# Performance work log

Measured on AMD Instinct MI355X. Metric: run time of the kernel, lower is better.

Reference implementation:

```python
import jax, jax.numpy as jnp
import numpy as np

B, T, D = 2, 4096, 1024
HD, HQ, KVH, W = 128, 8, 1, 1024   # head_dim, q_heads, kv_heads, window
HH, HG, K = 1536, 2048, 4          # hawk hidden, gmlp hidden, conv kernel
ALPHA_SCALE = float(np.log(8.0))   # alpha_log_scale (stored as log, used exp'd)


def setup_inputs() -> dict:
    key = jax.random.key(0)
    ks = jax.random.split(key, 16)
    n = lambda k, shape, std: jax.random.normal(k, shape, jnp.float32) * std
    return {
        'x': n(ks[0], (B, T, D), 1.0),
        'sn_g': jnp.ones((D,), jnp.float32),
        'q_w': n(ks[1], (HQ * HD, D), D ** -0.5),
        'kv_w': n(ks[2], (2 * KVH * HD, D), D ** -0.5),
        'ao_w': n(ks[3], (D, D), D ** -0.5),
        'sgn_g': jnp.ones((D,), jnp.float32),
        'sg_grow': n(ks[4], (2 * HG, D), D ** -0.5),
        'sg_shrink': n(ks[5], (D, HG), HG ** -0.5),
        'hn_g': jnp.ones((D,), jnp.float32),
        'h_in_w': n(ks[6], (2 * HH, D), D ** -0.5),
        'h_conv_w': n(ks[7], (HH, 1, K), K ** -0.5),
        'h_conv_b': jnp.zeros((HH,), jnp.float32),
        'h_gates_w': n(ks[8], (2 * HH, HH), HH ** -0.5),
        'h_gates_b': jnp.zeros((2 * HH,), jnp.float32),
        'h_forget': jnp.linspace(-4.323, -9.0, HH, dtype=jnp.float32),
        'h_out_w': n(ks[9], (D, HH), HH ** -0.5),
        'hgn_g': jnp.ones((D,), jnp.float32),
        'hg_grow': n(ks[10], (2 * HG, D), D ** -0.5),
        'hg_shrink': n(ks[11], (D, HG), HG ** -0.5),
    }


def rmsnorm(x, gamma):
    # original: gamma / dim**-0.5 * x / ||x||_2  (no eps)
    inv = jax.lax.rsqrt(jnp.sum(x * x, axis=-1, keepdims=True))
    return gamma * (x.shape[-1] ** 0.5) * x * inv


def rope(x, base=10000.0):
    # x: (B, T, H, HD); interleaved rotary over time axis 1
    t = x.shape[1]
    hd = x.shape[-1]
    inv = 1.0 / (base ** (jnp.arange(0, hd, 2, dtype=jnp.float32) / hd))
    ang = jnp.arange(t, dtype=jnp.float32)[:, None] * inv[None, :]  # (T, HD/2)
    cos = jnp.cos(ang)[None, :, None, :]
    sin = jnp.sin(ang)[None, :, None, :]
    x1, x2 = x[..., 0::2], x[..., 1::2]
    y1 = x1 * cos - x2 * sin
    y2 = x1 * sin + x2 * cos
    return jnp.stack([y1, y2], axis=-1).reshape(x.shape)


def sliding_mqa(x, q_w, kv_w, ao_w):
    # MQA with causal sliding window of W, computed in blocks of W
    q = (x @ q_w.T).reshape(B, T, HQ, HD)
    kv = (x @ kv_w.T).reshape(B, T, 2, KVH, HD)
    k = kv[:, :, 0, 0]  # (B, T, HD) since KVH == 1
    v = kv[:, :, 1, 0]
    q = rope(q)
    k = rope(k[:, :, None, :])[:, :, 0]
    nb = T // W
    qb = q.reshape(B, nb, W, HQ, HD)
    kb = k.reshape(B, nb, W, HD)
    vb = v.reshape(B, nb, W, HD)
    # prepend previous block (zeros for block 0)
    shift = lambda a: jnp.concatenate([jnp.zeros_like(a[:, :1]), a[:, :-1]], axis=1)
    k2 = jnp.concatenate([shift(kb), kb], axis=2)  # (B, nb, 2W, HD)
    v2 = jnp.concatenate([shift(vb), vb], axis=2)
    qi = jnp.arange(W)[:, None]
    kj = jnp.arange(2 * W)[None, :]
    base = (kj >= qi) & (kj <= qi + W)  # causal + window (i-j <= W)
    blk0 = base & (kj >= W)             # block 0 has no real previous block
    mask = jnp.where(jnp.arange(nb)[:, None, None] == 0, blk0[None], base[None])
    scores = jnp.einsum('bnqhd,bnkd->bhnqk', qb, k2) * (HD ** -0.5)
    scores = jnp.where(mask[None, None], scores, -jnp.inf)
    p = jax.nn.softmax(scores, axis=-1)
    o = jnp.einsum('bhnqk,bnkd->bnqhd', p, v2).reshape(B, T, HQ * HD)
    return o @ ao_w.T


def gated_mlp(x, grow_w, shrink_w):
    gate, h = jnp.split(x @ grow_w.T, 2, axis=-1)
    return (jax.nn.gelu(gate, approximate=False) * h) @ shrink_w.T


def hawk(x, in_w, conv_w, conv_b, gates_w, gates_b, forget_base, out_w):
    gate, u = jnp.split(x @ in_w.T, 2, axis=-1)  # (B, T, HH) each
    # depthwise causal conv1d (torch pads k-1 both sides then slices [:T])
    u_nch = jnp.transpose(u, (0, 2, 1))  # (B, HH, T)
    c = jax.lax.conv_general_dilated(
        u_nch, conv_w, window_strides=(1,), padding=[(K - 1, 0)],
        feature_group_count=HH, dimension_numbers=('NCH', 'OIH', 'NCH'))
    xc = jnp.transpose(c + conv_b[None, :, None], (0, 2, 1))  # (B, T, HH)
    fg, ig = jnp.split(xc @ gates_w.T + gates_b, 2, axis=-1)
    log_alpha = -np.exp(ALPHA_SCALE) * jax.nn.softplus(forget_base) * jax.nn.sigmoid(fg)
    alpha = jnp.exp(log_alpha)
    beta = jnp.sqrt(1.0 - alpha * alpha + 1e-6)
    xin = beta * jax.nn.sigmoid(ig) * xc
    # linear recurrence h_t = alpha_t * h_{t-1} + xin_t  via associative scan
    def combine(c1, c2):
        a1, x1 = c1
        a2, x2 = c2
        return a1 * a2, a2 * x1 + x2
    _, h = jax.lax.associative_scan(combine, (alpha, xin), axis=1)
    return (jax.nn.gelu(gate, approximate=False) * h) @ out_w.T


def reference(x, sn_g, q_w, kv_w, ao_w, sgn_g, sg_grow, sg_shrink,
              hn_g, h_in_w, h_conv_w, h_conv_b, h_gates_w, h_gates_b,
              h_forget, h_out_w, hgn_g, hg_grow, hg_shrink):
    x = x + sliding_mqa(rmsnorm(x, sn_g), q_w, kv_w, ao_w)
    x = x + gated_mlp(rmsnorm(x, sgn_g), sg_grow, sg_shrink)
    x = x + hawk(rmsnorm(x, hn_g), h_in_w, h_conv_w, h_conv_b,
                 h_gates_w, h_gates_b, h_forget, h_out_w)
    x = x + gated_mlp(rmsnorm(x, hgn_g), hg_grow, hg_shrink)
    return x
```

## Files before the change

### kernel.cpp

```cpp
#include <hip/hip_runtime.h>
#include <hip/hip_bf16.h>
#include <math.h>

#define B_  2
#define T_  4096
#define D_  1024
#define HD_ 128
#define HQ_ 8
#define W_  1024
#define HH_ 1536
#define HG_ 2048
#define KC_ 4

typedef float  f32x4  __attribute__((ext_vector_type(4)));
typedef float  f32x2  __attribute__((ext_vector_type(2)));
typedef __bf16 bf16x8 __attribute__((ext_vector_type(8)));
typedef unsigned short u16;
typedef unsigned short u16x2 __attribute__((ext_vector_type(2)));
typedef unsigned short u16x4 __attribute__((ext_vector_type(4)));
typedef unsigned short u16x8 __attribute__((ext_vector_type(8)));

__device__ __forceinline__ u16 f2bf(float f) {
    unsigned int u = __builtin_bit_cast(unsigned int, f);
    u += 0x7fffu + ((u >> 16) & 1u);
    return (u16)(u >> 16);
}
__device__ __forceinline__ float bf2f(u16 v) {
    unsigned int u = ((unsigned int)v) << 16;
    return __builtin_bit_cast(float, u);
}
__device__ __forceinline__ float gelu_exact(float x) {
    return 0.5f * x * (1.0f + erff(x * 0.70710678118654752f));
}
__device__ __forceinline__ float sigmoidf_(float x) {
    return 1.0f / (1.0f + expf(-x));
}

#define GLOAD16(gp, lp) __builtin_amdgcn_global_load_lds( \
    (const __attribute__((address_space(1))) void*)(gp),  \
    (__attribute__((address_space(3))) void*)(lp), 16, 0, 0)

struct CvtArgs {
    const float* src[10];
    u16* dst[10];
    long cum[11];
};
__global__ __launch_bounds__(256)
void cvt_all_kernel(CvtArgs a)
{
    long i = ((long)blockIdx.x * 256 + threadIdx.x) * 8;
    if (i >= a.cum[10]) return;
    int seg = 0;
#pragma unroll
    for (int s = 1; s < 10; s++) if (i >= a.cum[s]) seg = s;
    long off = i - a.cum[seg];
    const float* src = a.src[seg];
    u16* dst = a.dst[seg];
    f32x4 x = *(const f32x4*)(src + off);
    f32x4 y = *(const f32x4*)(src + off + 4);
    u16x4 ua, ub;
    ua.x = f2bf(x.x); ua.y = f2bf(x.y); ua.z = f2bf(x.z); ua.w = f2bf(x.w);
    ub.x = f2bf(y.x); ub.y = f2bf(y.y); ub.z = f2bf(y.z); ub.w = f2bf(y.w);
    *(u16x4*)(dst + off) = ua;
    *(u16x4*)(dst + off + 4) = ub;
}

template<int EPI, bool OBF>
__global__ __launch_bounds__(512)
void gemm_big_kernel(const u16* __restrict__ A, const u16* __restrict__ Bw,
                     const float* __restrict__ bias, const float* __restrict__ res,
                     const u16* gatebuf, void* outv,
                     int M, int N, int K)
{
    __shared__ u16 lA[3][256 * 32];
    __shared__ u16 lB[3][128 * 32];
    const int n0 = blockIdx.x * 128, m0 = blockIdx.y * 256;
    const int tid = threadIdx.x, w = tid >> 6, l = tid & 63;
    const int wr = w >> 1, wc = w & 1;
    const int lr = l & 15, lg = l >> 4;

    f32x4 acc[4][4];
#pragma unroll
    for (int i = 0; i < 4; i++)
#pragma unroll
        for (int j = 0; j < 4; j++) acc[i][j] = {0.f, 0.f, 0.f, 0.f};

    const int srow = tid >> 2;
    const int gslot = (((tid) & 3) - ((tid >> 3) & 3)) & 3;
    const u16* gA = A + (long)(m0 + srow) * K + gslot * 8;
    const u16* gB = Bw + (long)(n0 + srow) * K + gslot * 8;
    const int lofs = tid * 8;

#define STAGE_G(buf, kk)                                            \
    {                                                               \
        GLOAD16(gA + (kk),                 &lA[buf][lofs]);         \
        GLOAD16(gA + (long)128 * K + (kk), &lA[buf][4096 + lofs]);  \
        GLOAD16(gB + (kk),                 &lB[buf][lofs]);         \
    }

    const int NT = K >> 5;
    STAGE_G(0, 0);
    STAGE_G(1, 32);

    const int swzr = (lr >> 1) & 3;
    int cur = 0;
    for (int t = 0; t < NT; ++t) {
        if (t == NT - 1) { asm volatile("s_waitcnt vmcnt(0)" ::: "memory"); }
        else             { asm volatile("s_waitcnt vmcnt(3)" ::: "memory"); }
        __builtin_amdgcn_s_barrier();
        __builtin_amdgcn_sched_barrier(0);
        if (t + 2 < NT) {
            int nb = cur + 2; if (nb >= 3) nb -= 3;
            STAGE_G(nb, (t + 2) << 5);
        }
        bf16x8 af[4], bfr[4];
#pragma unroll
        for (int m = 0; m < 4; m++)
            af[m] = *(const bf16x8*)&lA[cur][(wr * 64 + m * 16 + lr) * 32 + (((lg + swzr) & 3) * 8)];
#pragma unroll
        for (int n = 0; n < 4; n++)
            bfr[n] = *(const bf16x8*)&lB[cur][(wc * 64 + n * 16 + lr) * 32 + (((lg + swzr) & 3) * 8)];
        __builtin_amdgcn_s_setprio(1);
#pragma unroll
        for (int m = 0; m < 4; m++)
#pragma unroll
            for (int n = 0; n < 4; n++)
                acc[m][n] = __builtin_amdgcn_mfma_f32_16x16x32_bf16(af[m], bfr[n], acc[m][n], 0, 0, 0);
        __builtin_amdgcn_s_setprio(0);
        cur++; if (cur == 3) cur = 0;
    }
#undef STAGE_G

#pragma unroll
    for (int m = 0; m < 4; m++)
#pragma unroll
        for (int n = 0; n < 4; n++) {
            const int col = n0 + wc * 64 + n * 16 + lr;
            const float bv = (EPI == 1) ? bias[col] : 0.f;
#pragma unroll
            for (int r = 0; r < 4; r++) {
                const int row = m0 + wr * 64 + m * 16 + lg * 4 + r;
                const long idx = (long)row * N + col;
                float v = acc[m][n][r] + bv;
                if (EPI == 2) v += res[idx];
                if (EPI == 3) v = gelu_exact(bf2f(gatebuf[idx])) * v;
                if (OBF) ((u16*)outv)[idx] = f2bf(v);
                else     ((float*)outv)[idx] = v;
            }
        }
}

template<int EPI, bool OBF>
__global__ __launch_bounds__(256)
void gemm_bf16_kernel(const u16* __restrict__ A, const u16* __restrict__ Bw,
                      const float* __restrict__ bias, const float* __restrict__ res,
                      const u16* gatebuf, void* outv,
                      int M, int N, int K)
{
    __shared__ u16 lA[3][128 * 32];
    __shared__ u16 lB[3][128 * 32];
    const int n0 = blockIdx.x * 128, m0 = blockIdx.y * 128;
    const int tid = threadIdx.x, w = tid >> 6, l = tid & 63;
    const int wr = w >> 1, wc = w & 1, lr = l & 15, lg = l >> 4;

    f32x4 acc[4][4];
#pragma unroll
    for (int i = 0; i < 4; i++)
#pragma unroll
        for (int j = 0; j < 4; j++) acc[i][j] = {0.f, 0.f, 0.f, 0.f};

    const int srow = w * 16 + (l >> 2);
    const int gslot = ((l & 3) - ((l >> 3) & 3)) & 3;
    const u16* gA = A + (long)(m0 + srow) * K + gslot * 8;
    const u16* gB = Bw + (long)(n0 + srow) * K + gslot * 8;
    const int lofs = w * 512 + l * 8;

#define STAGE_G(buf, kk)                                          \
    {                                                             \
        GLOAD16(gA + (kk),                &lA[buf][lofs]);        \
        GLOAD16(gA + (long)64 * K + (kk), &lA[buf][2048 + lofs]); \
        GLOAD16(gB + (kk),                &lB[buf][lofs]);        \
        GLOAD16(gB + (long)64 * K + (kk), &lB[buf][2048 + lofs]); \
    }

    const int NT = K >> 5;
    STAGE_G(0, 0);
    STAGE_G(1, 32);

    const int swzr = (lr >> 1) & 3;
    int cur = 0;
    for (int t = 0; t < NT; ++t) {
        if (t == NT - 1) { asm volatile("s_waitcnt vmcnt(0)" ::: "memory"); }
        else             { asm volatile("s_waitcnt vmcnt(4)" ::: "memory"); }
        __builtin_amdgcn_s_barrier();
        __builtin_amdgcn_sched_barrier(0);
        if (t + 2 < NT) {
            int nb = cur + 2; if (nb >= 3) nb -= 3;
            STAGE_G(nb, (t + 2) << 5);
        }
        bf16x8 af[4], bfr[4];
#pragma unroll
        for (int m = 0; m < 4; m++)
            af[m] = *(const bf16x8*)&lA[cur][(wr * 64 + m * 16 + lr) * 32 + (((lg + swzr) & 3) * 8)];
#pragma unroll
        for (int n = 0; n < 4; n++)
            bfr[n] = *(const bf16x8*)&lB[cur][(wc * 64 + n * 16 + lr) * 32 + (((lg + swzr) & 3) * 8)];
        __builtin_amdgcn_s_setprio(1);
#pragma unroll
        for (int m = 0; m < 4; m++)
#pragma unroll
            for (int n = 0; n < 4; n++)
                acc[m][n] = __builtin_amdgcn_mfma_f32_16x16x32_bf16(af[m], bfr[n], acc[m][n], 0, 0, 0);
        __builtin_amdgcn_s_setprio(0);
        cur++; if (cur == 3) cur = 0;
    }
#undef STAGE_G

#pragma unroll
    for (int m = 0; m < 4; m++)
#pragma unroll
        for (int n = 0; n < 4; n++) {
            const int col = n0 + wc * 64 + n * 16 + lr;
            const float bv = (EPI == 1) ? bias[col] : 0.f;
#pragma unroll
            for (int r = 0; r < 4; r++) {
                const int row = m0 + wr * 64 + m * 16 + lg * 4 + r;
                const long idx = (long)row * N + col;
                float v = acc[m][n][r] + bv;
                if (EPI == 2) v += res[idx];
                if (EPI == 3) v = gelu_exact(bf2f(gatebuf[idx])) * v;
                if (OBF) ((u16*)outv)[idx] = f2bf(v);
                else     ((float*)outv)[idx] = v;
            }
        }
}

__global__ __launch_bounds__(256)
void rmsnorm_kernel(const float* __restrict__ x, const float* __restrict__ g,
                    u16* __restrict__ out)
{
    const long row = blockIdx.x;
    const int tid = threadIdx.x;
    const float* xp = x + row * D_;
    f32x4 v = *(const f32x4*)(xp + tid * 4);
    float ss = v.x * v.x + v.y * v.y + v.z * v.z + v.w * v.w;
#pragma unroll
    for (int o = 1; o < 64; o <<= 1) ss += __shfl_xor(ss, o);
    __shared__ float ps[4];
    if ((tid & 63) == 0) ps[tid >> 6] = ss;
    __syncthreads();
    float tot = ps[0] + ps[1] + ps[2] + ps[3];
    float inv = rsqrtf(tot) * 32.0f;
    f32x4 gv = *(const f32x4*)(g + tid * 4);
    u16x4 o4;
    o4.x = f2bf(gv.x * v.x * inv); o4.y = f2bf(gv.y * v.y * inv);
    o4.z = f2bf(gv.z * v.z * inv); o4.w = f2bf(gv.w * v.w * inv);
    *(u16x4*)(out + row * D_ + tid * 4) = o4;
}

__global__ void rope_bf16_kernel(const float* __restrict__ q, const float* __restrict__ kv,
                                 u16* __restrict__ qb, u16* __restrict__ kb)
{
    const long NQ = (long)B_ * T_ * HQ_ * 64;
    const long NK = (long)B_ * T_ * 64;
    long idx = (long)blockIdx.x * blockDim.x + threadIdx.x;
    if (idx >= NQ + NK) return;
    int i; long t; const float* src; u16* dst;
    if (idx < NQ) {
        i = idx & 63;
        long bth = idx >> 6;
        t = (bth / HQ_) % T_;
        src = q + bth * HD_ + 2 * i;
        dst = qb + bth * HD_ + 2 * i;
    } else {
        long k = idx - NQ;
        i = k & 63;
        long bt = k >> 6;
        t = bt % T_;
        src = kv + bt * (2 * HD_) + 2 * i;
        dst = kb + bt * HD_ + 2 * i;
    }
    float freq = exp2f(-(float)i * 0.20762050593046014f);
    float ang = (float)t * freq;
    float sn, cs;
    sincosf(ang, &sn, &cs);
    f32x2 xv = *(const f32x2*)src;
    u16x2 yv;
    yv.x = f2bf(xv.x * cs - xv.y * sn);
    yv.y = f2bf(xv.x * sn + xv.y * cs);
    *(u16x2*)dst = yv;
}

__global__ __launch_bounds__(256)
void vtrans_kernel(const float* __restrict__ kv, u16* __restrict__ vt)
{
    __shared__ float tile[64][65];
    const int t0 = blockIdx.x * 64, d0 = blockIdx.y * 64, b = blockIdx.z;
    const int tid = threadIdx.x;
    {
        const int tl = tid & 63, dg = tid >> 6;
        const float* vp = kv + (((long)b * T_ + t0 + tl) * 2 + 1) * HD_ + d0 + dg * 16;
#pragma unroll
        for (int j = 0; j < 4; j++) {
            f32x4 v = *(const f32x4*)(vp + j * 4);
            tile[dg * 16 + j * 4 + 0][tl] = v.x;
            tile[dg * 16 + j * 4 + 1][tl] = v.y;
            tile[dg * 16 + j * 4 + 2][tl] = v.z;
            tile[dg * 16 + j * 4 + 3][tl] = v.w;
        }
    }
    __syncthreads();
    {
        const int dl = tid >> 2, tg = (tid & 3) * 16;
        u16x8 a, c;
#pragma unroll
        for (int j = 0; j < 8; j++) a[j] = f2bf(tile[dl][tg + j]);
#pragma unroll
        for (int j = 0; j < 8; j++) c[j] = f2bf(tile[dl][tg + 8 + j]);
        u16* dst = vt + ((long)b * HD_ + d0 + dl) * T_ + t0 + tg;
        *(u16x8*)dst = a;
        *(u16x8*)(dst + 8) = c;
    }
}

#define PLD 72

__global__ __launch_bounds__(256)
void attn_mfma3_kernel(const u16* __restrict__ qb, const u16* __restrict__ kb,
                       const u16* __restrict__ vt, u16* __restrict__ o)
{
    __shared__ u16 Ksh[2][64 * 128];
    __shared__ u16 Vsh[2][128 * 64];
    __shared__ u16 Psh[4 * 16 * PLD];

    const int qt = blockIdx.x, h = blockIdx.y, b = blockIdx.z;
    const int q0 = qt * 64;
    const int tid = threadIdx.x;
    const int w = tid >> 6, l = tid & 63;
    const int lr = l & 15, lg = l >> 4;

    bf16x8 qfr[4];
    {
        const u16* qp = qb + (((long)b * T_ + q0 + w * 16 + lr) * HQ_ + h) * HD_;
#pragma unroll
        for (int kt = 0; kt < 4; kt++)
            qfr[kt] = *(const bf16x8*)(qp + kt * 32 + lg * 8);
    }

    int oK[4], oV[4];
#pragma unroll
    for (int i = 0; i < 4; i++) {
        int krow = w * 16 + i * 4 + (l >> 4);
        int kc8 = (l & 15) ^ (krow & 7);
        oK[i] = krow * 128 + kc8 * 8;
        int vrow = w * 32 + i * 8 + (l >> 3);
        int vc8 = (l & 7) ^ (vrow & 7);
        oV[i] = vrow * T_ + vc8 * 8;
    }
    const u16* kbase = kb + (long)b * T_ * HD_;
    const u16* vbase = vt + (long)b * HD_ * T_;

    f32x4 oacc[8];
#pragma unroll
    for (int dt = 0; dt < 8; dt++) oacc[dt] = {0.f, 0.f, 0.f, 0.f};
    float mrun[4], srun[4];
#pragma unroll
    for (int r = 0; r < 4; r++) { mrun[r] = -1e30f; srun[r] = 0.f; }

    const int kt_lo = (q0 >= W_) ? (q0 - W_) : 0;
    const int nt = ((q0 - kt_lo) >> 6) + 1;
    const int sw = lr & 7;
    const float scale = 0.08838834764831845f;

#pragma unroll
    for (int i = 0; i < 4; i++) {
        GLOAD16(kbase + (long)kt_lo * HD_ + oK[i], &Ksh[0][w * 2048 + i * 512]);
        GLOAD16(vbase + kt_lo + oV[i], &Vsh[0][w * 2048 + i * 512]);
    }

    for (int t = 0; t < nt; ++t) {
        const int kt0 = kt_lo + t * 64;
        const int cur = t & 1;
        if (t + 1 < nt) {
            const int ktn = kt0 + 64;
#pragma unroll
            for (int i = 0; i < 4; i++) {
                GLOAD16(kbase + (long)ktn * HD_ + oK[i], &Ksh[cur ^ 1][w * 2048 + i * 512]);
                GLOAD16(vbase + ktn + oV[i], &Vsh[cur ^ 1][w * 2048 + i * 512]);
            }
            asm volatile("s_waitcnt vmcnt(8)" ::: "memory");
        } else {
            asm volatile("s_waitcnt vmcnt(0)" ::: "memory");
        }
        __builtin_amdgcn_s_barrier();
        __builtin_amdgcn_sched_barrier(0);

        const u16* Kc = Ksh[cur];
        const u16* Vc = Vsh[cur];

        f32x4 s[4];
        __builtin_amdgcn_s_setprio(1);
#pragma unroll
        for (int ct = 0; ct < 4; ct++) {
            s[ct] = {0.f, 0.f, 0.f, 0.f};
#pragma unroll
            for (int kt = 0; kt < 4; kt++) {
                bf16x8 kf = *(const bf16x8*)&Kc[(ct * 16 + lr) * 128 + (((kt * 4 + lg) ^ sw) * 8)];
                s[ct] = __builtin_amdgcn_mfma_f32_16x16x32_bf16(qfr[kt], kf, s[ct], 0, 0, 0);
            }
        }
        __builtin_amdgcn_s_setprio(0);

        float tmax[4] = {-3e38f, -3e38f, -3e38f, -3e38f};
        if (kt0 == q0) {
#pragma unroll
            for (int ct = 0; ct < 4; ct++) {
                const int kpos = kt0 + ct * 16 + lr;
#pragma unroll
                for (int r = 0; r < 4; r++) {
                    const int qpos = q0 + w * 16 + lg * 4 + r;
                    float v = s[ct][r] * scale;
                    v = (kpos <= qpos) ? v : -3e38f;
                    s[ct][r] = v;
                    tmax[r] = fmaxf(tmax[r], v);
                }
            }
        } else if (kt0 == q0 - W_) {
#pragma unroll
            for (int ct = 0; ct < 4; ct++) {
                const int kpos = kt0 + ct * 16 + lr;
#pragma unroll
                for (int r = 0; r < 4; r++) {
                    const int qpos = q0 + w * 16 + lg * 4 + r;
                    float v = s[ct][r] * scale;
                    v = (kpos + W_ >= qpos) ? v : -3e38f;
                    s[ct][r] = v;
                    tmax[r] = fmaxf(tmax[r], v);
                }
            }
        } else {
#pragma unroll
            for (int ct = 0; ct < 4; ct++)
#pragma unroll
                for (int r = 0; r < 4; r++) {
                    float v = s[ct][r] * scale;
                    s[ct][r] = v;
                    tmax[r] = fmaxf(tmax[r], v);
                }
        }
#pragma unroll
        for (int r = 0; r < 4; r++)
#pragma unroll
            for (int msk = 1; msk < 16; msk <<= 1)
                tmax[r] = fmaxf(tmax[r], __shfl_xor(tmax[r], msk));

        bool defer = (tmax[0] <= mrun[0] + 8.f) && (tmax[1] <= mrun[1] + 8.f) &&
                     (tmax[2] <= mrun[2] + 8.f) && (tmax[3] <= mrun[3] + 8.f);
        if (!__all(defer)) {
            float frv[4];
#pragma unroll
            for (int r = 0; r < 4; r++) {
                float mnew = fmaxf(mrun[r], tmax[r]);
                frv[r] = __expf(mrun[r] - mnew);
                mrun[r] = mnew;
                srun[r] *= frv[r];
            }
#pragma unroll
            for (int dt = 0; dt < 8; dt++) {
                oacc[dt][0] *= frv[0]; oacc[dt][1] *= frv[1];
                oacc[dt][2] *= frv[2]; oacc[dt][3] *= frv[3];
            }
        }

        u16* pw = &Psh[w * 16 * PLD];
        float psum[4] = {0.f, 0.f, 0.f, 0.f};
#pragma unroll
        for (int ct = 0; ct < 4; ct++)
#pragma unroll
            for (int r = 0; r < 4; r++) {
                float p = __expf(s[ct][r] - mrun[r]);
                psum[r] += p;
                pw[(lg * 4 + r) * PLD + ct * 16 + lr] = f2bf(p);
            }
#pragma unroll
        for (int r = 0; r < 4; r++) {
#pragma unroll
            for (int msk = 1; msk < 16; msk <<= 1)
                psum[r] += __shfl_xor(psum[r], msk);
            srun[r] += psum[r];
        }

        asm volatile("s_waitcnt lgkmcnt(0)" ::: "memory");
        bf16x8 pa0 = *(const bf16x8*)&pw[lr * PLD + lg * 8];
        bf16x8 pa1 = *(const bf16x8*)&pw[lr * PLD + 32 + lg * 8];
        __builtin_amdgcn_s_setprio(1);
#pragma unroll
        for (int dt = 0; dt < 8; dt++) {
            bf16x8 vf0 = *(const bf16x8*)&Vc[(dt * 16 + lr) * 64 + ((lg ^ sw) * 8)];
            bf16x8 vf1 = *(const bf16x8*)&Vc[(dt * 16 + lr) * 64 + (((4 + lg) ^ sw) * 8)];
            oacc[dt] = __builtin_amdgcn_mfma_f32_16x16x32_bf16(pa0, vf0, oacc[dt], 0, 0, 0);
            oacc[dt] = __builtin_amdgcn_mfma_f32_16x16x32_bf16(pa1, vf1, oacc[dt], 0, 0, 0);
        }
        __builtin_amdgcn_s_setprio(0);
        __syncthreads();
    }

#pragma unroll
    for (int r = 0; r < 4; r++) {
        const int qpos = q0 + w * 16 + lg * 4 + r;
        float inv = 1.f / srun[r];
        u16* op = o + ((long)b * T_ + qpos) * (HQ_ * HD_) + h * HD_;
#pragma unroll
        for (int dt = 0; dt < 8; dt++)
            op[dt * 16 + lr] = f2bf(oacc[dt][r] * inv);
    }
}

__global__ void conv_kernel(const u16* __restrict__ u, const float* __restrict__ w,
                            const float* __restrict__ bias, u16* __restrict__ xc)
{
    long idx = (long)blockIdx.x * blockDim.x + threadIdx.x;
    if (idx >= (long)B_ * T_ * HH_) return;
    int ch = (int)(idx % HH_);
    long row = idx / HH_;
    int t = (int)(row % T_);
    float acc = bias[ch];
#pragma unroll
    for (int k = 0; k < KC_; k++) {
        int ts = t - 3 + k;
        if (ts >= 0) acc += bf2f(u[(row - t + ts) * HH_ + ch]) * w[ch * KC_ + k];
    }
    xc[idx] = f2bf(acc);
}

#define CS_ 64
#define NC_ (T_ / CS_)

__device__ __forceinline__ void alpha_xin(const u16 fg, const u16 ig, const u16 xc,
                                          float sp, float& a, float& xin)
{
    a = expf(-8.0f * sp * sigmoidf_(bf2f(fg)));
    xin = sqrtf(1.f - a * a + 1e-6f) * sigmoidf_(bf2f(ig)) * bf2f(xc);
}

__global__ void scan1_kernel(const u16* __restrict__ fg, const u16* __restrict__ ig,
                             const u16* __restrict__ xc, const float* __restrict__ fb,
                             float* __restrict__ P, float* __restrict__ L)
{
    long idx = (long)blockIdx.x * blockDim.x + threadIdx.x;
    if (idx >= (long)B_ * NC_ * HH_) return;
    int ch = (int)(idx % HH_);
    int chunk = (int)((idx / HH_) % NC_);
    int b = (int)(idx / ((long)HH_ * NC_));
    long base = ((long)b * T_ + chunk * CS_) * HH_ + ch;
    float f = fb[ch];
    float sp = (f > 20.f) ? f : log1pf(expf(f));
    float p = 1.f, lacc = 0.f;
    for (int i = 0; i < CS_; i++) {
        long o = base + (long)i * HH_;
        float a, xin;
        alpha_xin(fg[o], ig[o], xc[o], sp, a, xin);
        lacc = a * lacc + xin;
        p *= a;
    }
    P[idx] = p; L[idx] = lacc;
}
__global__ void scan2_kernel(const float* __restrict__ P, const float* __restrict__ L,
                             float* __restrict__ I)
{
    long idx = (long)blockIdx.x * blockDim.x + threadIdx.x;
    if (idx >= (long)B_ * HH_) return;
    int ch = (int)(idx % HH_);
    int b = (int)(idx / HH_);
    float init = 0.f;
    for (int c = 0; c < NC_; c++) {
        long o = ((long)b * NC_ + c) * HH_ + ch;
        I[o] = init;
        init = P[o] * init + L[o];
    }
}
__global__ void scan3_kernel(const u16* __restrict__ fg, const u16* __restrict__ ig,
                             const u16* __restrict__ xc, const float* __restrict__ fb,
                             const float* __restrict__ I, const u16* __restrict__ gate,
                             u16* __restrict__ glu)
{
    long idx = (long)blockIdx.x * blockDim.x + threadIdx.x;
    if (idx >= (long)B_ * NC_ * HH_) return;
    int ch = (int)(idx % HH_);
    int chunk = (int)((idx / HH_) % NC_);
    int b = (int)(idx / ((long)HH_ * NC_));
    long base = ((long)b * T_ + chunk * CS_) * HH_ + ch;
    float f = fb[ch];
    float sp = (f > 20.f) ? f : log1pf(expf(f));
    float h = I[idx];
    for (int i = 0; i < CS_; i++) {
        long o = base + (long)i * HH_;
        float a, xin;
        alpha_xin(fg[o], ig[o], xc[o], sp, a, xin);
        h = a * h + xin;
        glu[o] = f2bf(gelu_exact(bf2f(gate[o])) * h);
    }
}

static inline long cdivl(long a, long b) { return (a + b - 1) / b; }

extern "C" void kernel_launch(void* const* d_in, const int* in_sizes, int n_in,
                              void* d_out, int out_size, void* d_ws, size_t ws_size,
                              hipStream_t stream)
{
    const float* x_in   = (const float*)d_in[0];
    const float* sn_g   = (const float*)d_in[1];
    const float* q_w    = (const float*)d_in[2];
    const float* kv_w   = (const float*)d_in[3];
    const float* ao_w   = (const float*)d_in[4];
    const float* sgn_g  = (const float*)d_in[5];
    const float* sg_grow   = (const float*)d_in[6];
    const float* sg_shrink = (const float*)d_in[7];
    const float* hn_g   = (const float*)d_in[8];
    const float* h_in_w = (const float*)d_in[9];
    const float* h_conv_w = (const float*)d_in[10];
    const float* h_conv_b = (const float*)d_in[11];
    const float* h_gates_w = (const float*)d_in[12];
    const float* h_gates_b = (const float*)d_in[13];
    const float* h_forget  = (const float*)d_in[14];
    const float* h_out_w   = (const float*)d_in[15];
    const float* hgn_g  = (const float*)d_in[16];
    const float* hg_grow   = (const float*)d_in[17];
    const float* hg_shrink = (const float*)d_in[18];
    float* out = (float*)d_out;

    char* wsb = (char*)d_ws;
    u16* Wq  = (u16*)wsb;
    u16* Wkv = Wq  + 1048576;
    u16* Wao = Wkv + 262144;
    u16* Wsg = Wao + 1048576;
    u16* Wss = Wsg + 4194304;
    u16* Whi = Wss + 2097152;
    u16* Whg = Whi + 3145728;
    u16* Who = Whg + 4718592;
    u16* Wgg = Who + 1572864;
    u16* Wgs = Wgg + 4194304;
    char* ab = wsb + 48758784;
    u16*   XN   = (u16*)(ab + 0);
    char*  S2   = ab + 16777216;
    char*  S3   = ab + 50331648;
    char*  S4   = ab + 75497472;
    char*  S5   = ab + 100663296;
    char*  S6   = ab + 125829120;
    float* PB   = (float*)(ab + 150994944);
    float* LB   = (float*)(ab + 151781376);
    float* IB   = (float*)(ab + 152567808);

    const long M = (long)B_ * T_;
    dim3 blk(256);
    dim3 blk5(512);
    const float* NULF = nullptr;
    const u16*   NULB = nullptr;

    {
        CvtArgs ca;
        const float* srcs[10] = {q_w, kv_w, ao_w, sg_grow, sg_shrink,
                                 h_in_w, h_gates_w, h_out_w, hg_grow, hg_shrink};
        u16* dsts[10] = {Wq, Wkv, Wao, Wsg, Wss, Whi, Whg, Who, Wgg, Wgs};
        long ns[10] = {1048576, 262144, 1048576, 4194304, 2097152,
                       3145728, 4718592, 1572864, 4194304, 2097152};
        long cum = 0;
        for (int i = 0; i < 10; i++) {
            ca.src[i] = srcs[i]; ca.dst[i] = dsts[i]; ca.cum[i] = cum; cum += ns[i];
        }
        ca.cum[10] = cum;
        cvt_all_kernel<<<dim3(cdivl(cum / 8, 256)), blk, 0, stream>>>(ca);
    }

    {
        float* Q  = (float*)S2;
        float* KV = (float*)S3;
        u16*   Kb = (u16*)(S3 + 8388608);
        u16*   Vt = (u16*)(S3 + 10485760);
        u16*   Qb = (u16*)S4;
        u16*   AT = (u16*)S5;
        rmsnorm_kernel<<<dim3(M), blk, 0, stream>>>(x_in, sn_g, XN);
        gemm_big_kernel<0,false><<<dim3(8, 32), blk5, 0, stream>>>(XN, Wq, NULF, NULF, NULB, Q, M, 1024, 1024);
        gemm_bf16_kernel<0,false><<<dim3(2, 64), blk, 0, stream>>>(XN, Wkv, NULF, NULF, NULB, KV, M, 256, 1024);
        rope_bf16_kernel<<<dim3(cdivl((long)B_ * T_ * (HQ_ + 1) * 64, 256)), blk, 0, stream>>>(Q, KV, Qb, Kb);
        vtrans_kernel<<<dim3(T_ / 64, 2, B_), blk, 0, stream>>>(KV, Vt);
        attn_mfma3_kernel<<<dim3(T_ / 64, HQ_, B_), blk, 0, stream>>>(Qb, Kb, Vt, AT);
        gemm_big_kernel<2,false><<<dim3(8, 32), blk5, 0, stream>>>(AT, Wao, NULF, x_in, NULB, out, M, 1024, 1024);
    }

    {
        u16* GATE = (u16*)S2;
        rmsnorm_kernel<<<dim3(M), blk, 0, stream>>>(out, sgn_g, XN);
        gemm_big_kernel<0,true><<<dim3(16, 32), blk5, 0, stream>>>(XN, Wsg, NULF, NULF, NULB, GATE, M, 2048, 1024);
        gemm_big_kernel<3,true><<<dim3(16, 32), blk5, 0, stream>>>(XN, Wsg + (size_t)2048 * 1024, NULF, NULF, GATE, GATE, M, 2048, 1024);
        gemm_big_kernel<2,false><<<dim3(8, 32), blk5, 0, stream>>>(GATE, Wss, NULF, out, NULB, out, M, 1024, 2048);
    }

    {
        u16* GATEH = (u16*)S2;
        u16* U     = (u16*)S3;
        u16* XC    = (u16*)S4;
        u16* FG    = (u16*)S5;
        u16* IG    = (u16*)S6;
        rmsnorm_kernel<<<dim3(M), blk, 0, stream>>>(out, hn_g, XN);
        gemm_big_kernel<0,true><<<dim3(12, 32), blk5, 0, stream>>>(XN, Whi, NULF, NULF, NULB, GATEH, M, 1536, 1024);
        gemm_big_kernel<0,true><<<dim3(12, 32), blk5, 0, stream>>>(XN, Whi + (size_t)1536 * 1024, NULF, NULF, NULB, U, M, 1536, 1024);
        conv_kernel<<<dim3(cdivl(M * HH_, 256)), blk, 0, stream>>>(U, h_conv_w, h_conv_b, XC);
        gemm_big_kernel<1,true><<<dim3(12, 32), blk5, 0, stream>>>(XC, Whg, h_gates_b, NULF, NULB, FG, M, 1536, 1536);
        gemm_big_kernel<1,true><<<dim3(12, 32), blk5, 0, stream>>>(XC, Whg + (size_t)1536 * 1536, h_gates_b + 1536, NULF, NULB, IG, M, 1536, 1536);
        scan1_kernel<<<dim3(cdivl((long)B_ * NC_ * HH_, 256)), blk, 0, stream>>>(FG, IG, XC, h_forget, PB, LB);
        scan2_kernel<<<dim3(cdivl((long)B_ * HH_, 256)), blk, 0, stream>>>(PB, LB, IB);
        scan3_kernel<<<dim3(cdivl((long)B_ * NC_ * HH_, 256)), blk, 0, stream>>>(FG, IG, XC, h_forget, IB, GATEH, U);
        gemm_big_kernel<2,false><<<dim3(8, 32), blk5, 0, stream>>>(U, Who, NULF, out, NULB, out, M, 1024, 1536);
    }

    {
        u16* GLU = (u16*)S2;
        rmsnorm_kernel<<<dim3(M), blk, 0, stream>>>(out, hgn_g, XN);
        gemm_big_kernel<0,true><<<dim3(16, 32), blk5, 0, stream>>>(XN, Wgg, NULF, NULF, NULB, GLU, M, 2048, 1024);
        gemm_big_kernel<3,true><<<dim3(16, 32), blk5, 0, stream>>>(XN, Wgg + (size_t)2048 * 1024, NULF, NULF, GLU, GLU, M, 2048, 1024);
        gemm_big_kernel<2,false><<<dim3(8, 32), blk5, 0, stream>>>(GLU, Wgs, NULF, out, NULB, out, M, 1024, 2048);
    }
}
```

Baseline: 1.049 ms.

## Double GEMM K-tile to 64 with XOR swizzle; use smaller GEMM for hawk projections

```diff
diff --git a/kernel.cpp b/kernel.cpp
--- a/kernel.cpp
+++ b/kernel.cpp
@@ -67,13 +67,13 @@
 
 template<int EPI, bool OBF>
 __global__ __launch_bounds__(512)
-void gemm_big_kernel(const u16* __restrict__ A, const u16* __restrict__ Bw,
-                     const float* __restrict__ bias, const float* __restrict__ res,
-                     const u16* gatebuf, void* outv,
-                     int M, int N, int K)
-{
-    __shared__ u16 lA[3][256 * 32];
-    __shared__ u16 lB[3][128 * 32];
+void gemm_big64_kernel(const u16* __restrict__ A, const u16* __restrict__ Bw,
+                       const float* __restrict__ bias, const float* __restrict__ res,
+                       const u16* gatebuf, void* outv,
+                       int M, int N, int K)
+{
+    __shared__ u16 lA[3][256 * 64];
+    __shared__ u16 lB[3][128 * 64];
     const int n0 = blockIdx.x * 128, m0 = blockIdx.y * 256;
     const int tid = threadIdx.x, w = tid >> 6, l = tid & 63;
     const int wr = w >> 1, wc = w & 1;
@@ -85,48 +85,54 @@
 #pragma unroll
         for (int j = 0; j < 4; j++) acc[i][j] = {0.f, 0.f, 0.f, 0.f};
 
-    const int srow = tid >> 2;
-    const int gslot = (((tid) & 3) - ((tid >> 3) & 3)) & 3;
+    const int srow = tid >> 3;
+    const int gslot = (tid & 7) ^ ((tid >> 3) & 7);
     const u16* gA = A + (long)(m0 + srow) * K + gslot * 8;
     const u16* gB = Bw + (long)(n0 + srow) * K + gslot * 8;
     const int lofs = tid * 8;
 
-#define STAGE_G(buf, kk)                                            \
-    {                                                               \
-        GLOAD16(gA + (kk),                 &lA[buf][lofs]);         \
-        GLOAD16(gA + (long)128 * K + (kk), &lA[buf][4096 + lofs]);  \
-        GLOAD16(gB + (kk),                 &lB[buf][lofs]);         \
-    }
-
-    const int NT = K >> 5;
+#define STAGE_G(buf, kk)                                              \
+    {                                                                 \
+        GLOAD16(gA + (kk),                 &lA[buf][lofs]);           \
+        GLOAD16(gA + (long)64 * K + (kk),  &lA[buf][4096 + lofs]);    \
+        GLOAD16(gA + (long)128 * K + (kk), &lA[buf][8192 + lofs]);    \
+        GLOAD16(gA + (long)192 * K + (kk), &lA[buf][12288 + lofs]);   \
+        GLOAD16(gB + (kk),                 &lB[buf][lofs]);           \
+        GLOAD16(gB + (long)64 * K + (kk),  &lB[buf][4096 + lofs]);    \
+    }
+
+    const int NT = K >> 6;
     STAGE_G(0, 0);
-    STAGE_G(1, 32);
-
-    const int swzr = (lr >> 1) & 3;
+    STAGE_G(1, 64);
+
+    const int swz = lr & 7;
     int cur = 0;
     for (int t = 0; t < NT; ++t) {
         if (t == NT - 1) { asm volatile("s_waitcnt vmcnt(0)" ::: "memory"); }
-        else             { asm volatile("s_waitcnt vmcnt(3)" ::: "memory"); }
+        else             { asm volatile("s_waitcnt vmcnt(6)" ::: "memory"); }
         __builtin_amdgcn_s_barrier();
         __builtin_amdgcn_sched_barrier(0);
         if (t + 2 < NT) {
             int nb = cur + 2; if (nb >= 3) nb -= 3;
-            STAGE_G(nb, (t + 2) << 5);
-        }
-        bf16x8 af[4], bfr[4];
-#pragma unroll
-        for (int m = 0; m < 4; m++)
-            af[m] = *(const bf16x8*)&lA[cur][(wr * 64 + m * 16 + lr) * 32 + (((lg + swzr) & 3) * 8)];
-#pragma unroll
-        for (int n = 0; n < 4; n++)
-            bfr[n] = *(const bf16x8*)&lB[cur][(wc * 64 + n * 16 + lr) * 32 + (((lg + swzr) & 3) * 8)];
-        __builtin_amdgcn_s_setprio(1);
-#pragma unroll
-        for (int m = 0; m < 4; m++)
+            STAGE_G(nb, (t + 2) << 6);
+        }
+#pragma unroll
+        for (int ks = 0; ks < 2; ks++) {
+            bf16x8 af[4], bfr[4];
+#pragma unroll
+            for (int m = 0; m < 4; m++)
+                af[m] = *(const bf16x8*)&lA[cur][(wr * 64 + m * 16 + lr) * 64 + (((ks * 4 + lg) ^ swz) * 8)];
 #pragma unroll
             for (int n = 0; n < 4; n++)
-                acc[m][n] = __builtin_amdgcn_mfma_f32_16x16x32_bf16(af[m], bfr[n], acc[m][n], 0, 0, 0);
-        __builtin_amdgcn_s_setprio(0);
+                bfr[n] = *(const bf16x8*)&lB[cur][(wc * 64 + n * 16 + lr) * 64 + (((ks * 4 + lg) ^ swz) * 8)];
+            __builtin_amdgcn_s_setprio(1);
+#pragma unroll
+            for (int m = 0; m < 4; m++)
+#pragma unroll
+                for (int n = 0; n < 4; n++)
+                    acc[m][n] = __builtin_amdgcn_mfma_f32_16x16x32_bf16(af[m], bfr[n], acc[m][n], 0, 0, 0);
+            __builtin_amdgcn_s_setprio(0);
+        }
         cur++; if (cur == 3) cur = 0;
     }
 #undef STAGE_G
@@ -680,20 +686,20 @@
         u16*   Qb = (u16*)S4;
         u16*   AT = (u16*)S5;
         rmsnorm_kernel<<<dim3(M), blk, 0, stream>>>(x_in, sn_g, XN);
-        gemm_big_kernel<0,false><<<dim3(8, 32), blk5, 0, stream>>>(XN, Wq, NULF, NULF, NULB, Q, M, 1024, 1024);
+        gemm_big64_kernel<0,false><<<dim3(8, 32), blk5, 0, stream>>>(XN, Wq, NULF, NULF, NULB, Q, M, 1024, 1024);
         gemm_bf16_kernel<0,false><<<dim3(2, 64), blk, 0, stream>>>(XN, Wkv, NULF, NULF, NULB, KV, M, 256, 1024);
         rope_bf16_kernel<<<dim3(cdivl((long)B_ * T_ * (HQ_ + 1) * 64, 256)), blk, 0, stream>>>(Q, KV, Qb, Kb);
         vtrans_kernel<<<dim3(T_ / 64, 2, B_), blk, 0, stream>>>(KV, Vt);
         attn_mfma3_kernel<<<dim3(T_ / 64, HQ_, B_), blk, 0, stream>>>(Qb, Kb, Vt, AT);
-        gemm_big_kernel<2,false><<<dim3(8, 32), blk5, 0, stream>>>(AT, Wao, NULF, x_in, NULB, out, M, 1024, 1024);
+        gemm_big64_kernel<2,false><<<dim3(8, 32), blk5, 0, stream>>>(AT, Wao, NULF, x_in, NULB, out, M, 1024, 1024);
     }
 
     {
         u16* GATE = (u16*)S2;
         rmsnorm_kernel<<<dim3(M), blk, 0, stream>>>(out, sgn_g, XN);
-        gemm_big_kernel<0,true><<<dim3(16, 32), blk5, 0, stream>>>(XN, Wsg, NULF, NULF, NULB, GATE, M, 2048, 1024);
-        gemm_big_kernel<3,true><<<dim3(16, 32), blk5, 0, stream>>>(XN, Wsg + (size_t)2048 * 1024, NULF, NULF, GATE, GATE, M, 2048, 1024);
-        gemm_big_kernel<2,false><<<dim3(8, 32), blk5, 0, stream>>>(GATE, Wss, NULF, out, NULB, out, M, 1024, 2048);
+        gemm_big64_kernel<0,true><<<dim3(16, 32), blk5, 0, stream>>>(XN, Wsg, NULF, NULF, NULB, GATE, M, 2048, 1024);
+        gemm_big64_kernel<3,true><<<dim3(16, 32), blk5, 0, stream>>>(XN, Wsg + (size_t)2048 * 1024, NULF, NULF, GATE, GATE, M, 2048, 1024);
+        gemm_big64_kernel<2,false><<<dim3(8, 32), blk5, 0, stream>>>(GATE, Wss, NULF, out, NULB, out, M, 1024, 2048);
     }
 
     {
@@ -703,22 +709,22 @@
         u16* FG    = (u16*)S5;
         u16* IG    = (u16*)S6;
         rmsnorm_kernel<<<dim3(M), blk, 0, stream>>>(out, hn_g, XN);
-        gemm_big_kernel<0,true><<<dim3(12, 32), blk5, 0, stream>>>(XN, Whi, NULF, NULF, NULB, GATEH, M, 1536, 1024);
-        gemm_big_kernel<0,true><<<dim3(12, 32), blk5, 0, stream>>>(XN, Whi + (size_t)1536 * 1024, NULF, NULF, NULB, U, M, 1536, 1024);
+        gemm_bf16_kernel<0,true><<<dim3(12, 64), blk, 0, stream>>>(XN, Whi, NULF, NULF, NULB, GATEH, M, 1536, 1024);
+        gemm_bf16_kernel<0,true><<<dim3(12, 64), blk, 0, stream>>>(XN, Whi + (size_t)1536 * 1024, NULF, NULF, NULB, U, M, 1536, 1024);
         conv_kernel<<<dim3(cdivl(M * HH_, 256)), blk, 0, stream>>>(U, h_conv_w, h_conv_b, XC);
-        gemm_big_kernel<1,true><<<dim3(12, 32), blk5, 0, stream>>>(XC, Whg, h_gates_b, NULF, NULB, FG, M, 1536, 1536);
-        gemm_big_kernel<1,true><<<dim3(12, 32), blk5, 0, stream>>>(XC, Whg + (size_t)1536 * 1536, h_gates_b + 1536, NULF, NULB, IG, M, 1536, 1536);
+        gemm_bf16_kernel<1,true><<<dim3(12, 64), blk, 0, stream>>>(XC, Whg, h_gates_b, NULF, NULB, FG, M, 1536, 1536);
+        gemm_bf16_kernel<1,true><<<dim3(12, 64), blk, 0, stream>>>(XC, Whg + (size_t)1536 * 1536, h_gates_b + 1536, NULF, NULB, IG, M, 1536, 1536);
         scan1_kernel<<<dim3(cdivl((long)B_ * NC_ * HH_, 256)), blk, 0, stream>>>(FG, IG, XC, h_forget, PB, LB);
         scan2_kernel<<<dim3(cdivl((long)B_ * HH_, 256)), blk, 0, stream>>>(PB, LB, IB);
         scan3_kernel<<<dim3(cdivl((long)B_ * NC_ * HH_, 256)), blk, 0, stream>>>(FG, IG, XC, h_forget, IB, GATEH, U);
-        gemm_big_kernel<2,false><<<dim3(8, 32), blk5, 0, stream>>>(U, Who, NULF, out, NULB, out, M, 1024, 1536);
+        gemm_big64_kernel<2,false><<<dim3(8, 32), blk5, 0, stream>>>(U, Who, NULF, out, NULB, out, M, 1024, 1536);
     }
 
     {
         u16* GLU = (u16*)S2;
         rmsnorm_kernel<<<dim3(M), blk, 0, stream>>>(out, hgn_g, XN);
-        gemm_big_kernel<0,true><<<dim3(16, 32), blk5, 0, stream>>>(XN, Wgg, NULF, NULF, NULB, GLU, M, 2048, 1024);
-        gemm_big_kernel<3,true><<<dim3(16, 32), blk5, 0, stream>>>(XN, Wgg + (size_t)2048 * 1024, NULF, NULF, GLU, GLU, M, 2048, 1024);
-        gemm_big_kernel<2,false><<<dim3(8, 32), blk5, 0, stream>>>(GLU, Wgs, NULF, out, NULB, out, M, 1024, 2048);
-    }
-}
+        gemm_big64_kernel<0,true><<<dim3(16, 32), blk5, 0, stream>>>(XN, Wgg, NULF, NULF, NULB, GLU, M, 2048, 1024);
+        gemm_big64_kernel<3,true><<<dim3(16, 32), blk5, 0, stream>>>(XN, Wgg + (size_t)2048 * 1024, NULF, NULF, GLU, GLU, M, 2048, 1024);
+        gemm_big64_kernel<2,false><<<dim3(8, 32), blk5, 0, stream>>>(GLU, Wgs, NULF, out, NULB, out, M, 1024, 2048);
+    }
+}
```

After: 1.085 ms. 3.4% more time.

## Share K/V tiles across two query blocks in attention; use smaller GEMM for hawk

Applied to the files above, without the earlier changes.

```diff
diff --git a/kernel.cpp b/kernel.cpp
--- a/kernel.cpp
+++ b/kernel.cpp
@@ -325,8 +325,122 @@
 
 #define PLD 72
 
+__device__ __forceinline__ void attn_tile_process(
+    const int kt0, const int qb0, const int w, const int lr, const int lg,
+    const u16* __restrict__ Kc, const u16* __restrict__ Vc, u16* __restrict__ pw,
+    const bf16x8* qfr, float* mrun, float* srun, f32x4* oacc)
+{
+    const int sw = lr & 7;
+    const float scale = 0.08838834764831845f;
+
+    f32x4 s[4];
+    __builtin_amdgcn_s_setprio(1);
+#pragma unroll
+    for (int ct = 0; ct < 4; ct++) {
+        s[ct] = {0.f, 0.f, 0.f, 0.f};
+#pragma unroll
+        for (int kt = 0; kt < 4; kt++) {
+            bf16x8 kf = *(const bf16x8*)&Kc[(ct * 16 + lr) * 128 + (((kt * 4 + lg) ^ sw) * 8)];
+            s[ct] = __builtin_amdgcn_mfma_f32_16x16x32_bf16(qfr[kt], kf, s[ct], 0, 0, 0);
+        }
+    }
+    __builtin_amdgcn_s_setprio(0);
+
+    float tmax[4] = {-3e38f, -3e38f, -3e38f, -3e38f};
+    if (kt0 == qb0) {
+#pragma unroll
+        for (int ct = 0; ct < 4; ct++) {
+            const int kpos = kt0 + ct * 16 + lr;
+#pragma unroll
+            for (int r = 0; r < 4; r++) {
+                const int qpos = qb0 + w * 16 + lg * 4 + r;
+                float v = s[ct][r] * scale;
+                v = (kpos <= qpos) ? v : -3e38f;
+                s[ct][r] = v;
+                tmax[r] = fmaxf(tmax[r], v);
+            }
+        }
+    } else if (kt0 == qb0 - W_) {
+#pragma unroll
+        for (int ct = 0; ct < 4; ct++) {
+            const int kpos = kt0 + ct * 16 + lr;
+#pragma unroll
+            for (int r = 0; r < 4; r++) {
+                const int qpos = qb0 + w * 16 + lg * 4 + r;
+                float v = s[ct][r] * scale;
+                v = (kpos + W_ >= qpos) ? v : -3e38f;
+                s[ct][r] = v;
+                tmax[r] = fmaxf(tmax[r], v);
+            }
+        }
+    } else {
+#pragma unroll
+        for (int ct = 0; ct < 4; ct++)
+#pragma unroll
+            for (int r = 0; r < 4; r++) {
+                float v = s[ct][r] * scale;
+                s[ct][r] = v;
+                tmax[r] = fmaxf(tmax[r], v);
+            }
+    }
+#pragma unroll
+    for (int r = 0; r < 4; r++)
+#pragma unroll
+        for (int msk = 1; msk < 16; msk <<= 1)
+            tmax[r] = fmaxf(tmax[r], __shfl_xor(tmax[r], msk));
+
+    bool defer = (tmax[0] <= mrun[0] + 8.f) && (tmax[1] <= mrun[1] + 8.f) &&
+                 (tmax[2] <= mrun[2] + 8.f) && (tmax[3] <= mrun[3] + 8.f);
+    if (!__all(defer)) {
+        float frv[4];
+#pragma unroll
+        for (int r = 0; r < 4; r++) {
+            float mnew = fmaxf(mrun[r], tmax[r]);
+            frv[r] = __expf(mrun[r] - mnew);
+            mrun[r] = mnew;
+            srun[r] *= frv[r];
+        }
+#pragma unroll
+        for (int dt = 0; dt < 8; dt++) {
+            oacc[dt][0] *= frv[0]; oacc[dt][1] *= frv[1];
+            oacc[dt][2] *= frv[2]; oacc[dt][3] *= frv[3];
+        }
+    }
+
+    asm volatile("s_waitcnt lgkmcnt(0)" ::: "memory");
+    float psum[4] = {0.f, 0.f, 0.f, 0.f};
+#pragma unroll
+    for (int ct = 0; ct < 4; ct++)
+#pragma unroll
+        for (int r = 0; r < 4; r++) {
+            float p = __expf(s[ct][r] - mrun[r]);
+            psum[r] += p;
+            pw[(lg * 4 + r) * PLD + ct * 16 + lr] = f2bf(p);
+        }
+#pragma unroll
+    for (int r = 0; r < 4; r++) {
+#pragma unroll
+        for (int msk = 1; msk < 16; msk <<= 1)
+            psum[r] += __shfl_xor(psum[r], msk);
+        srun[r] += psum[r];
+    }
+
+    asm volatile("s_waitcnt lgkmcnt(0)" ::: "memory");
+    bf16x8 pa0 = *(const bf16x8*)&pw[lr * PLD + lg * 8];
+    bf16x8 pa1 = *(const bf16x8*)&pw[lr * PLD + 32 + lg * 8];
+    __builtin_amdgcn_s_setprio(1);
+#pragma unroll
+    for (int dt = 0; dt < 8; dt++) {
+        bf16x8 vf0 = *(const bf16x8*)&Vc[(dt * 16 + lr) * 64 + ((lg ^ sw) * 8)];
+        bf16x8 vf1 = *(const bf16x8*)&Vc[(dt * 16 + lr) * 64 + (((4 + lg) ^ sw) * 8)];
+        oacc[dt] = __builtin_amdgcn_mfma_f32_16x16x32_bf16(pa0, vf0, oacc[dt], 0, 0, 0);
+        oacc[dt] = __builtin_amdgcn_mfma_f32_16x16x32_bf16(pa1, vf1, oacc[dt], 0, 0, 0);
+    }
+    __builtin_amdgcn_s_setprio(0);
+}
+
 __global__ __launch_bounds__(256)
-void attn_mfma3_kernel(const u16* __restrict__ qb, const u16* __restrict__ kb,
+void attn_mfma5_kernel(const u16* __restrict__ qb, const u16* __restrict__ kb,
                        const u16* __restrict__ vt, u16* __restrict__ o)
 {
     __shared__ u16 Ksh[2][64 * 128];
@@ -334,17 +448,20 @@
     __shared__ u16 Psh[4 * 16 * PLD];
 
     const int qt = blockIdx.x, h = blockIdx.y, b = blockIdx.z;
-    const int q0 = qt * 64;
+    const int Q0 = qt * 128;
     const int tid = threadIdx.x;
     const int w = tid >> 6, l = tid & 63;
     const int lr = l & 15, lg = l >> 4;
 
-    bf16x8 qfr[4];
+    bf16x8 qfrA[4], qfrB[4];
     {
-        const u16* qp = qb + (((long)b * T_ + q0 + w * 16 + lr) * HQ_ + h) * HD_;
-#pragma unroll
-        for (int kt = 0; kt < 4; kt++)
-            qfr[kt] = *(const bf16x8*)(qp + kt * 32 + lg * 8);
+        const u16* qpA = qb + (((long)b * T_ + Q0 + w * 16 + lr) * HQ_ + h) * HD_;
+        const u16* qpB = qpA + (long)64 * HQ_ * HD_;
+#pragma unroll
+        for (int kt = 0; kt < 4; kt++) {
+            qfrA[kt] = *(const bf16x8*)(qpA + kt * 32 + lg * 8);
+            qfrB[kt] = *(const bf16x8*)(qpB + kt * 32 + lg * 8);
+        }
     }
 
     int oK[4], oV[4];
@@ -360,17 +477,19 @@
     const u16* kbase = kb + (long)b * T_ * HD_;
     const u16* vbase = vt + (long)b * HD_ * T_;
 
-    f32x4 oacc[8];
-#pragma unroll
-    for (int dt = 0; dt < 8; dt++) oacc[dt] = {0.f, 0.f, 0.f, 0.f};
-    float mrun[4], srun[4];
-#pragma unroll
-    for (int r = 0; r < 4; r++) { mrun[r] = -1e30f; srun[r] = 0.f; }
-
-    const int kt_lo = (q0 >= W_) ? (q0 - W_) : 0;
-    const int nt = ((q0 - kt_lo) >> 6) + 1;
-    const int sw = lr & 7;
-    const float scale = 0.08838834764831845f;
+    f32x4 oaccA[8], oaccB[8];
+#pragma unroll
+    for (int dt = 0; dt < 8; dt++) { oaccA[dt] = {0.f,0.f,0.f,0.f}; oaccB[dt] = {0.f,0.f,0.f,0.f}; }
+    float mrunA[4], srunA[4], mrunB[4], srunB[4];
+#pragma unroll
+    for (int r = 0; r < 4; r++) {
+        mrunA[r] = -1e30f; srunA[r] = 0.f;
+        mrunB[r] = -1e30f; srunB[r] = 0.f;
+    }
+
+    const int kt_lo = (Q0 >= W_) ? (Q0 - W_) : 0;
+    const int kt_hi = Q0 + 64;
+    const int nt = ((kt_hi - kt_lo) >> 6) + 1;
 
 #pragma unroll
     for (int i = 0; i < 4; i++) {
@@ -378,6 +497,7 @@
         GLOAD16(vbase + kt_lo + oV[i], &Vsh[0][w * 2048 + i * 512]);
     }
 
+    u16* pw = &Psh[w * 16 * PLD];
     for (int t = 0; t < nt; ++t) {
         const int kt0 = kt_lo + t * 64;
         const int cur = t & 1;
@@ -398,121 +518,26 @@
         const u16* Kc = Ksh[cur];
         const u16* Vc = Vsh[cur];
 
-        f32x4 s[4];
-        __builtin_amdgcn_s_setprio(1);
-#pragma unroll
-        for (int ct = 0; ct < 4; ct++) {
-            s[ct] = {0.f, 0.f, 0.f, 0.f};
-#pragma unroll
-            for (int kt = 0; kt < 4; kt++) {
-                bf16x8 kf = *(const bf16x8*)&Kc[(ct * 16 + lr) * 128 + (((kt * 4 + lg) ^ sw) * 8)];
-                s[ct] = __builtin_amdgcn_mfma_f32_16x16x32_bf16(qfr[kt], kf, s[ct], 0, 0, 0);
-            }
-        }
-        __builtin_amdgcn_s_setprio(0);
-
-        float tmax[4] = {-3e38f, -3e38f, -3e38f, -3e38f};
-        if (kt0 == q0) {
-#pragma unroll
-            for (int ct = 0; ct < 4; ct++) {
-                const int kpos = kt0 + ct * 16 + lr;
-#pragma unroll
-                for (int r = 0; r < 4; r++) {
-                    const int qpos = q0 + w * 16 + lg * 4 + r;
-                    float v = s[ct][r] * scale;
-                    v = (kpos <= qpos) ? v : -3e38f;
-                    s[ct][r] = v;
-                    tmax[r] = fmaxf(tmax[r], v);
-                }
-            }
-        } else if (kt0 == q0 - W_) {
-#pragma unroll
-            for (int ct = 0; ct < 4; ct++) {
-                const int kpos = kt0 + ct * 16 + lr;
-#pragma unroll
-                for (int r = 0; r < 4; r++) {
-                    const int qpos = q0 + w * 16 + lg * 4 + r;
-                    float v = s[ct][r] * scale;
-                    v = (kpos + W_ >= qpos) ? v : -3e38f;
-                    s[ct][r] = v;
-                    tmax[r] = fmaxf(tmax[r], v);
-                }
-            }
-        } else {
-#pragma unroll
-            for (int ct = 0; ct < 4; ct++)
-#pragma unroll
-                for (int r = 0; r < 4; r++) {
-                    float v = s[ct][r] * scale;
-                    s[ct][r] = v;
-                    tmax[r] = fmaxf(tmax[r], v);
-                }
-        }
-#pragma unroll
-        for (int r = 0; r < 4; r++)
-#pragma unroll
-            for (int msk = 1; msk < 16; msk <<= 1)
-                tmax[r] = fmaxf(tmax[r], __shfl_xor(tmax[r], msk));
-
-        bool defer = (tmax[0] <= mrun[0] + 8.f) && (tmax[1] <= mrun[1] + 8.f) &&
-                     (tmax[2] <= mrun[2] + 8.f) && (tmax[3] <= mrun[3] + 8.f);
-        if (!__all(defer)) {
-            float frv[4];
-#pragma unroll
-            for (int r = 0; r < 4; r++) {
-                float mnew = fmaxf(mrun[r], tmax[r]);
-                frv[r] = __expf(mrun[r] - mnew);
-                mrun[r] = mnew;
-                srun[r] *= frv[r];
-            }
-#pragma unroll
-            for (int dt = 0; dt < 8; dt++) {
-                oacc[dt][0] *= frv[0]; oacc[dt][1] *= frv[1];
-                oacc[dt][2] *= frv[2]; oacc[dt][3] *= frv[3];
-            }
-        }
-
-        u16* pw = &Psh[w * 16 * PLD];
-        float psum[4] = {0.f, 0.f, 0.f, 0.f};
-#pragma unroll
-        for (int ct = 0; ct < 4; ct++)
-#pragma unroll
-            for (int r = 0; r < 4; r++) {
-                float p = __expf(s[ct][r] - mrun[r]);
-                psum[r] += p;
-                pw[(lg * 4 + r) * PLD + ct * 16 + lr] = f2bf(p);
-            }
-#pragma unroll
-        for (int r = 0; r < 4; r++) {
-#pragma unroll
-            for (int msk = 1; msk < 16; msk <<= 1)
-                psum[r] += __shfl_xor(psum[r], msk);
-            srun[r] += psum[r];
-        }
-
-        asm volatile("s_waitcnt lgkmcnt(0)" ::: "memory");
-        bf16x8 pa0 = *(const bf16x8*)&pw[lr * PLD + lg * 8];
-        bf16x8 pa1 = *(const bf16x8*)&pw[lr * PLD + 32 + lg * 8];
-        __builtin_amdgcn_s_setprio(1);
+        if (kt0 <= Q0)
+            attn_tile_process(kt0, Q0, w, lr, lg, Kc, Vc, pw, qfrA, mrunA, srunA, oaccA);
+        if (kt0 >= Q0 + 64 - W_)
+            attn_tile_process(kt0, Q0 + 64, w, lr, lg, Kc, Vc, pw, qfrB, mrunB, srunB, oaccB);
+
+        __syncthreads();
+    }
+
+#pragma unroll
+    for (int r = 0; r < 4; r++) {
+        const int qposA = Q0 + w * 16 + lg * 4 + r;
+        float invA = 1.f / srunA[r];
+        u16* opA = o + ((long)b * T_ + qposA) * (HQ_ * HD_) + h * HD_;
+        float invB = 1.f / srunB[r];
+        u16* opB = opA + (long)64 * (HQ_ * HD_);
 #pragma unroll
         for (int dt = 0; dt < 8; dt++) {
-            bf16x8 vf0 = *(const bf16x8*)&Vc[(dt * 16 + lr) * 64 + ((lg ^ sw) * 8)];
-            bf16x8 vf1 = *(const bf16x8*)&Vc[(dt * 16 + lr) * 64 + (((4 + lg) ^ sw) * 8)];
-            oacc[dt] = __builtin_amdgcn_mfma_f32_16x16x32_bf16(pa0, vf0, oacc[dt], 0, 0, 0);
-            oacc[dt] = __builtin_amdgcn_mfma_f32_16x16x32_bf16(pa1, vf1, oacc[dt], 0, 0, 0);
-        }
-        __builtin_amdgcn_s_setprio(0);
-        __syncthreads();
-    }
-
-#pragma unroll
-    for (int r = 0; r < 4; r++) {
-        const int qpos = q0 + w * 16 + lg * 4 + r;
-        float inv = 1.f / srun[r];
-        u16* op = o + ((long)b * T_ + qpos) * (HQ_ * HD_) + h * HD_;
-#pragma unroll
-        for (int dt = 0; dt < 8; dt++)
-            op[dt * 16 + lr] = f2bf(oacc[dt][r] * inv);
+            opA[dt * 16 + lr] = f2bf(oaccA[dt][r] * invA);
+            opB[dt * 16 + lr] = f2bf(oaccB[dt][r] * invB);
+        }
     }
 }
 
@@ -684,7 +709,7 @@
         gemm_bf16_kernel<0,false><<<dim3(2, 64), blk, 0, stream>>>(XN, Wkv, NULF, NULF, NULB, KV, M, 256, 1024);
         rope_bf16_kernel<<<dim3(cdivl((long)B_ * T_ * (HQ_ + 1) * 64, 256)), blk, 0, stream>>>(Q, KV, Qb, Kb);
         vtrans_kernel<<<dim3(T_ / 64, 2, B_), blk, 0, stream>>>(KV, Vt);
-        attn_mfma3_kernel<<<dim3(T_ / 64, HQ_, B_), blk, 0, stream>>>(Qb, Kb, Vt, AT);
+        attn_mfma5_kernel<<<dim3(T_ / 128, HQ_, B_), blk, 0, stream>>>(Qb, Kb, Vt, AT);
         gemm_big_kernel<2,false><<<dim3(8, 32), blk5, 0, stream>>>(AT, Wao, NULF, x_in, NULB, out, M, 1024, 1024);
     }
 
@@ -703,11 +728,11 @@
         u16* FG    = (u16*)S5;
         u16* IG    = (u16*)S6;
         rmsnorm_kernel<<<dim3(M), blk, 0, stream>>>(out, hn_g, XN);
-        gemm_big_kernel<0,true><<<dim3(12, 32), blk5, 0, stream>>>(XN, Whi, NULF, NULF, NULB, GATEH, M, 1536, 1024);
-        gemm_big_kernel<0,true><<<dim3(12, 32), blk5, 0, stream>>>(XN, Whi + (size_t)1536 * 1024, NULF, NULF, NULB, U, M, 1536, 1024);
+        gemm_bf16_kernel<0,true><<<dim3(12, 64), blk, 0, stream>>>(XN, Whi, NULF, NULF, NULB, GATEH, M, 1536, 1024);
+        gemm_bf16_kernel<0,true><<<dim3(12, 64), blk, 0, stream>>>(XN, Whi + (size_t)1536 * 1024, NULF, NULF, NULB, U, M, 1536, 1024);
         conv_kernel<<<dim3(cdivl(M * HH_, 256)), blk, 0, stream>>>(U, h_conv_w, h_conv_b, XC);
-        gemm_big_kernel<1,true><<<dim3(12, 32), blk5, 0, stream>>>(XC, Whg, h_gates_b, NULF, NULB, FG, M, 1536, 1536);
-        gemm_big_kernel<1,true><<<dim3(12, 32), blk5, 0, stream>>>(XC, Whg + (size_t)1536 * 1536, h_gates_b + 1536, NULF, NULB, IG, M, 1536, 1536);
+        gemm_bf16_kernel<1,true><<<dim3(12, 64), blk, 0, stream>>>(XC, Whg, h_gates_b, NULF, NULB, FG, M, 1536, 1536);
+        gemm_bf16_kernel<1,true><<<dim3(12, 64), blk, 0, stream>>>(XC, Whg + (size_t)1536 * 1536, h_gates_b + 1536, NULF, NULB, IG, M, 1536, 1536);
         scan1_kernel<<<dim3(cdivl((long)B_ * NC_ * HH_, 256)), blk, 0, stream>>>(FG, IG, XC, h_forget, PB, LB);
         scan2_kernel<<<dim3(cdivl((long)B_ * HH_, 256)), blk, 0, stream>>>(PB, LB, IB);
         scan3_kernel<<<dim3(cdivl((long)B_ * NC_ * HH_, 256)), blk, 0, stream>>>(FG, IG, XC, h_forget, IB, GATEH, U);
```

Result: slower. 1.074 ms (+2.3%).
